# Kernel tuning notes

Hardware: AMD Instinct MI355X
Metric: run time of the kernel (lower is better)

## Reference

```python
import jax, jax.numpy as jnp
import numpy as np

B, L, D = 4, 1024, 512
H, DH = 8, 64
E = 65536  # total subgraph node entries
BN_EPS = 1e-5


def setup_inputs() -> dict:
    key = jax.random.key(0)
    ks = jax.random.split(key, 16)
    x = jax.random.normal(ks[0], (B, L, D), dtype=jnp.float32)
    lattice = jax.random.normal(ks[1], (B, 6), dtype=jnp.float32)  # unused (cond_dim=0)
    B_graph = jax.random.normal(ks[2], (B, L, L), dtype=jnp.float32) * 0.02
    N = B * L
    subgraph_node_index = jax.random.randint(ks[3], (E,), 0, N, dtype=jnp.int32)
    subgraph_indicator = jnp.sort(jax.random.randint(ks[4], (E,), 0, N, dtype=jnp.int32))
    attn_mask = jnp.triu(jnp.ones((L, L), dtype=bool), k=1)  # True = masked (causal)
    s = 0.02
    # Linear weights stored as [in, out]
    Wq = jax.random.normal(ks[5], (D, H * DH), jnp.float32) * s
    Wk = jax.random.normal(ks[6], (D, H * DH), jnp.float32) * s
    Wv = jax.random.normal(ks[7], (D, H * DH), jnp.float32) * s
    Wo = jax.random.normal(ks[8], (H * DH, D), jnp.float32) * s
    bq = jnp.zeros((H * DH,), jnp.float32)
    bk = jnp.zeros((H * DH,), jnp.float32)
    bv = jnp.zeros((H * DH,), jnp.float32)
    bo = jnp.zeros((D,), jnp.float32)
    Wmp = jax.random.normal(ks[9], (D, D), jnp.float32) * s
    bmp = jnp.zeros((D,), jnp.float32)
    bn_gamma = jnp.ones((2 * D,), jnp.float32)
    bn_beta = jnp.zeros((2 * D,), jnp.float32)
    Wex = jax.random.normal(ks[10], (2 * D, D), jnp.float32) * s
    bex = jnp.zeros((D,), jnp.float32)
    struct_scale = jnp.zeros((1,), jnp.float32) + 0.1  # nonzero so bias path is exercised
    return dict(x=x, lattice=lattice, B_graph=B_graph,
                subgraph_node_index=subgraph_node_index,
                subgraph_indicator=subgraph_indicator, attn_mask=attn_mask,
                Wq=Wq, bq=bq, Wk=Wk, bk=bk, Wv=Wv, bv=bv, Wo=Wo, bo=bo,
                Wmp=Wmp, bmp=bmp, bn_gamma=bn_gamma, bn_beta=bn_beta,
                Wex=Wex, bex=bex, struct_scale=struct_scale)


def _extractor(x_flat, sub_idx, sub_ind, Wmp, bmp, bn_gamma, bn_beta, Wex, bex):
    N = x_flat.shape[0]
    x_sub = x_flat[sub_idx]                       # [E, D]
    h = x_sub + (x_sub @ Wmp + bmp)               # 1 message-passing layer (residual)
    # scatter_mean over subgraph_indicator, dim_size=N
    sums = jax.ops.segment_sum(h, sub_ind, num_segments=N)
    cnt = jax.ops.segment_sum(jnp.ones((h.shape[0],), h.dtype), sub_ind, num_segments=N)
    h_pool = sums / jnp.maximum(cnt, 1.0)[:, None]
    out = jnp.concatenate([x_flat, h_pool], axis=-1)  # [N, 2D]
    # BatchNorm1d (training-mode batch stats)
    mu = jnp.mean(out, axis=0)
    var = jnp.var(out, axis=0)
    out = (out - mu) * jax.lax.rsqrt(var + BN_EPS) * bn_gamma + bn_beta
    return out @ Wex + bex                        # [N, D]


def reference(x, lattice, B_graph, subgraph_node_index, subgraph_indicator, attn_mask,
              Wq, bq, Wk, bk, Wv, bv, Wo, bo, Wmp, bmp, bn_gamma, bn_beta,
              Wex, bex, struct_scale):
    Bb, Ll, Dd = x.shape
    scale = 1.0 / np.sqrt(DH).astype(np.float32)
    q = (x @ Wq + bq).reshape(Bb, Ll, H, DH).transpose(0, 2, 1, 3)
    k = (x @ Wk + bk).reshape(Bb, Ll, H, DH).transpose(0, 2, 1, 3)
    v = (x @ Wv + bv).reshape(Bb, Ll, H, DH).transpose(0, 2, 1, 3)
    scores = jnp.einsum('bhqd,bhkd->bhqk', q, k) * scale
    # structural bias from GNN extractor
    x_flat = x.reshape(Bb * Ll, Dd)
    ex = _extractor(x_flat, subgraph_node_index, subgraph_indicator,
                    Wmp, bmp, bn_gamma, bn_beta, Wex, bex)
    x_struct = ex.reshape(Bb, Ll, Dd)
    K = jnp.einsum('bqd,bkd->bqk', x_struct, x_struct) / np.sqrt(Dd).astype(np.float32)
    scores = scores + struct_scale[0] * K[:, None]
    scores = scores + B_graph[:, None]
    mask = attn_mask[None, None]                  # (1,1,L,L), True = masked
    scores = jnp.where(mask, jnp.float32(-10000.0), scores)
    attn = jax.nn.softmax(scores.astype(jnp.float32), axis=-1).astype(scores.dtype)
    # dropout is identity (eval / p effectively 0)
    out = jnp.einsum('bhqk,bhkd->bhqd', attn, v)
    out = out.transpose(0, 2, 1, 3).reshape(Bb, Ll, H * DH)
    out = out @ Wo + bo
    return out, attn
```

## Files before the change

kernel.cpp:

```cpp
#include <hip/hip_runtime.h>
#include <math.h>

#define BB 4
#define LL 1024
#define DD 512
#define HH 8
#define DHH 64
#define EE 65536
#define NNODES 4096
#define HD 512
#define TWO_D 1024

typedef short bf16x8 __attribute__((ext_vector_type(8)));
typedef short short4v __attribute__((ext_vector_type(4)));
typedef float f32x4 __attribute__((ext_vector_type(4)));
typedef unsigned int u32;
#define GL_AS __attribute__((address_space(1)))
#define LDS_AS __attribute__((address_space(3)))

__device__ __forceinline__ short f2bf(float f) {
  u32 u = __builtin_bit_cast(u32, f);
  u = (u + 0x7fffu + ((u >> 16) & 1u)) >> 16;
  return (short)u;
}
__device__ __forceinline__ float b2f(short s) {
  u32 u = ((u32)(unsigned short)s) << 16;
  return __builtin_bit_cast(float, u);
}
__device__ __forceinline__ void gload_lds16(const short* g, short* l) {
  __builtin_amdgcn_global_load_lds((GL_AS const u32*)g, (LDS_AS u32*)l, 16, 0, 0);
}

template <int ROWS>
__device__ __forceinline__ void stage32(const short* g, int lda, short* lds, int tid) {
  const int w = tid >> 6, l = tid & 63;
#pragma unroll
  for (int rep = 0; rep < ROWS / 64; ++rep) {
    const int rbase = rep * 64 + w * 16;
    gload_lds16(g + (size_t)(rbase + (l >> 2)) * lda + (l & 3) * 8, lds + rbase * 32);
  }
}

template <int MREP, int NREP>
__device__ __forceinline__ void mfma_step(const short* As, const short* Bs, int lds_ld, int kofs,
                                          f32x4 (&acc)[MREP][NREP], int wr, int wc, int l) {
  bf16x8 a[MREP], b[NREP];
#pragma unroll
  for (int mi = 0; mi < MREP; ++mi) {
    const int row = wr * (MREP * 16) + mi * 16 + (l & 15);
    a[mi] = *(const bf16x8*)(As + row * lds_ld + kofs + ((l >> 4) << 3));
  }
#pragma unroll
  for (int ni = 0; ni < NREP; ++ni) {
    const int row = wc * (NREP * 16) + ni * 16 + (l & 15);
    b[ni] = *(const bf16x8*)(Bs + row * lds_ld + kofs + ((l >> 4) << 3));
  }
#pragma unroll
  for (int mi = 0; mi < MREP; ++mi)
#pragma unroll
    for (int ni = 0; ni < NREP; ++ni)
      acc[mi][ni] = __builtin_amdgcn_mfma_f32_16x16x32_bf16(a[mi], b[ni], acc[mi][ni], 0, 0, 0);
}

template <int ROWB>
__device__ __forceinline__ bf16x8 ldsw(const short* base, int row, int bir) {
  const int bo = (row * ROWB + bir) ^ ((row & 7) << 4);
  return *(const bf16x8*)((const char*)base + bo);
}

__global__ __launch_bounds__(256) void k_cast_x(const float* __restrict__ x, short* __restrict__ xb) {
  const int i = (blockIdx.x * 256 + threadIdx.x) * 8;
  float4 f0 = *(const float4*)(x + i), f1 = *(const float4*)(x + i + 4);
  bf16x8 s;
  s[0] = f2bf(f0.x); s[1] = f2bf(f0.y); s[2] = f2bf(f0.z); s[3] = f2bf(f0.w);
  s[4] = f2bf(f1.x); s[5] = f2bf(f1.y); s[6] = f2bf(f1.z); s[7] = f2bf(f1.w);
  *(bf16x8*)(xb + i) = s;
}

__global__ __launch_bounds__(256) void k_tcast5(const float* __restrict__ Wq, const float* __restrict__ Wk,
                                                const float* __restrict__ Wv, const float* __restrict__ Wmp,
                                                const float* __restrict__ Wo,
                                                short* __restrict__ WcatT, short* __restrict__ WoT) {
  __shared__ float t[32][33];
  const int zz = blockIdx.z;
  const float* W = (zz == 0) ? Wq : (zz == 1) ? Wk : (zz == 2) ? Wv : (zz == 3) ? Wmp : Wo;
  short* out = (zz < 4) ? (WcatT + zz * 512 * 512) : WoT;
  const int k0 = blockIdx.y * 32, n0 = blockIdx.x * 32;
  const int tx = threadIdx.x, ty = threadIdx.y;
#pragma unroll
  for (int i = 0; i < 4; ++i)
    t[ty + 8 * i][tx] = W[(size_t)(k0 + ty + 8 * i) * 512 + n0 + tx];
  __syncthreads();
#pragma unroll
  for (int i = 0; i < 4; ++i)
    out[(size_t)(n0 + ty + 8 * i) * 512 + k0 + tx] = f2bf(t[tx][ty + 8 * i]);
}

__global__ __launch_bounds__(256) void k_tcast(const float* __restrict__ W, short* __restrict__ out,
                                               int K, int N) {
  __shared__ float t[32][33];
  const int k0 = blockIdx.y * 32, n0 = blockIdx.x * 32;
  const int tx = threadIdx.x, ty = threadIdx.y;
#pragma unroll
  for (int i = 0; i < 4; ++i)
    t[ty + 8 * i][tx] = W[(size_t)(k0 + ty + 8 * i) * N + n0 + tx];
  __syncthreads();
#pragma unroll
  for (int i = 0; i < 4; ++i)
    out[(size_t)(n0 + ty + 8 * i) * K + k0 + tx] = f2bf(t[tx][ty + 8 * i]);
}

__global__ __launch_bounds__(256) void k_pack_bias(const float* bq, const float* bk,
                                                   const float* bv, const float* bmp,
                                                   float* __restrict__ bcat) {
  const int i = blockIdx.x * 256 + threadIdx.x;
  const float* src = (i < 512) ? bq : (i < 1024) ? bk : (i < 1536) ? bv : bmp;
  bcat[i] = src[i & 511];
}

__global__ __launch_bounds__(256) void k_gemm_qkvg(const short* __restrict__ A,
                                                   const short* __restrict__ Bw,
                                                   const float* __restrict__ bcat,
                                                   const float* __restrict__ x,
                                                   short* __restrict__ qT, short* __restrict__ kT,
                                                   short* __restrict__ vT, short* __restrict__ g_bf) {
  __shared__ __align__(16) short As[128 * 32];
  __shared__ __align__(16) short Bs[128 * 32];
  const int tid = threadIdx.x, l = tid & 63, w = tid >> 6, wr = w >> 1, wc = w & 1;
  const int m0 = blockIdx.y * 128, n0 = blockIdx.x * 128;
  f32x4 acc[4][4] = {};
  for (int k0 = 0; k0 < 512; k0 += 32) {
    stage32<128>(A + (size_t)m0 * 512 + k0, 512, As, tid);
    stage32<128>(Bw + (size_t)n0 * 512 + k0, 512, Bs, tid);
    __syncthreads();
    mfma_step<4, 4>(As, Bs, 32, 0, acc, wr, wc, l);
    __syncthreads();
  }
  const int lr = l >> 4, lc = l & 15;
#pragma unroll
  for (int mi = 0; mi < 4; ++mi)
#pragma unroll
    for (int ni = 0; ni < 4; ++ni) {
      const int col = n0 + wc * 64 + ni * 16 + lc;
      const int which = col >> 9;
#pragma unroll
      for (int r = 0; r < 4; ++r) {
        const int row = m0 + wr * 64 + mi * 16 + lr * 4 + r;
        float v = acc[mi][ni][r] + bcat[col];
        if (which < 3) {
          const int hh = (col >> 6) & 7, dh = col & 63;
          const int bb = row >> 10, ll2 = row & 1023;
          short* dst = (which == 0) ? qT : (which == 1) ? kT : vT;
          dst[((size_t)((bb * 8 + hh) * 1024 + ll2)) * 64 + dh] = f2bf(v);
        } else {
          const int c = col & 511;
          g_bf[(size_t)row * 512 + c] = f2bf(v + x[(size_t)row * 512 + c]);
        }
      }
    }
}

__global__ __launch_bounds__(256) void k_gemm_ex(const short* __restrict__ A,
                                                 const short* __restrict__ Bw,
                                                 const float* __restrict__ bias,
                                                 short* __restrict__ C) {
  __shared__ __align__(16) short As[64 * 32];
  __shared__ __align__(16) short Bs[128 * 32];
  const int tid = threadIdx.x, l = tid & 63, w = tid >> 6, wr = w >> 1, wc = w & 1;
  const int m0 = blockIdx.y * 64, n0 = blockIdx.x * 128;
  f32x4 acc[2][4] = {};
  for (int k0 = 0; k0 < 1024; k0 += 32) {
    stage32<64>(A + (size_t)m0 * 1024 + k0, 1024, As, tid);
    stage32<128>(Bw + (size_t)n0 * 1024 + k0, 1024, Bs, tid);
    __syncthreads();
    mfma_step<2, 4>(As, Bs, 32, 0, acc, wr, wc, l);
    __syncthreads();
  }
  const int lr = l >> 4, lc = l & 15;
#pragma unroll
  for (int mi = 0; mi < 2; ++mi)
#pragma unroll
    for (int ni = 0; ni < 4; ++ni) {
      const int col = n0 + wc * 64 + ni * 16 + lc;
      const float bv = bias[col];
#pragma unroll
      for (int r = 0; r < 4; ++r) {
        const int row = m0 + wr * 32 + mi * 16 + lr * 4 + r;
        C[(size_t)row * 512 + col] = f2bf(acc[mi][ni][r] + bv);
      }
    }
}

__global__ __launch_bounds__(256) void k_gemm_oproj(const short* __restrict__ A,
                                                    const short* __restrict__ Bw,
                                                    const float* __restrict__ bias,
                                                    float* __restrict__ C) {
  __shared__ __align__(16) short As[64 * 32];
  __shared__ __align__(16) short Bs[128 * 32];
  const int tid = threadIdx.x, l = tid & 63, w = tid >> 6, wr = w >> 1, wc = w & 1;
  const int m0 = blockIdx.y * 64, n0 = blockIdx.x * 128;
  f32x4 acc[2][4] = {};
  for (int k0 = 0; k0 < 512; k0 += 32) {
    stage32<64>(A + (size_t)m0 * 512 + k0, 512, As, tid);
    stage32<128>(Bw + (size_t)n0 * 512 + k0, 512, Bs, tid);
    __syncthreads();
    mfma_step<2, 4>(As, Bs, 32, 0, acc, wr, wc, l);
    __syncthreads();
  }
  const int lr = l >> 4, lc = l & 15;
#pragma unroll
  for (int mi = 0; mi < 2; ++mi)
#pragma unroll
    for (int ni = 0; ni < 4; ++ni) {
      const int col = n0 + wc * 64 + ni * 16 + lc;
      const float bv = bias[col];
#pragma unroll
      for (int r = 0; r < 4; ++r) {
        const int row = m0 + wr * 32 + mi * 16 + lr * 4 + r;
        C[(size_t)row * 512 + col] = acc[mi][ni][r] + bv;
      }
    }
}

__global__ __launch_bounds__(256) void k_kstruct(const short* __restrict__ ex,
                                                 const float* __restrict__ Bg,
                                                 const float* __restrict__ ssp,
                                                 float* __restrict__ Ksc) {
  const int mt = blockIdx.y, nt = blockIdx.x, b = blockIdx.z;
  if (nt > mt) return;
  __shared__ __align__(16) short As[128 * 32];
  __shared__ __align__(16) short Bs[128 * 32];
  const int tid = threadIdx.x, l = tid & 63, w = tid >> 6, wr = w >> 1, wc = w & 1;
  const int m0 = mt * 128, n0 = nt * 128;
  const short* Az = ex + (size_t)b * 1024 * 512;
  f32x4 acc[4][4] = {};
  for (int k0 = 0; k0 < 512; k0 += 32) {
    stage32<128>(Az + (size_t)m0 * 512 + k0, 512, As, tid);
    stage32<128>(Az + (size_t)n0 * 512 + k0, 512, Bs, tid);
    __syncthreads();
    mfma_step<4, 4>(As, Bs, 32, 0, acc, wr, wc, l);
    __syncthreads();
  }
  const float sc = ssp[0] * 0.04419417382415922f;
  const float* Bgb = Bg + (size_t)b * 1024 * 1024;
  float* Kb = Ksc + (size_t)b * 1024 * 1024;
  const int lr = l >> 4, lc = l & 15;
#pragma unroll
  for (int mi = 0; mi < 4; ++mi)
#pragma unroll
    for (int ni = 0; ni < 4; ++ni) {
      const int col = n0 + wc * 64 + ni * 16 + lc;
#pragma unroll
      for (int r = 0; r < 4; ++r) {
        const int row = m0 + wr * 64 + mi * 16 + lr * 4 + r;
        Kb[(size_t)row * 1024 + col] = fmaf(acc[mi][ni][r], sc, Bgb[(size_t)row * 1024 + col]);
      }
    }
}

__global__ __launch_bounds__(256) void k_attn(const short* __restrict__ qT,
                                              const short* __restrict__ kT,
                                              const short* __restrict__ vT,
                                              const float* __restrict__ Ksc,
                                              float* __restrict__ attn,
                                              short* __restrict__ o_bf) {
  __shared__ __align__(16) short Qs[64 * 64];
  __shared__ __align__(16) short Ks[128 * 64];
  __shared__ __align__(16) short Ps[64 * 128];
  __shared__ __align__(16) short Vls[64 * 128];
  __shared__ float mred[2][64], sred[2][64];

  const int tid = threadIdx.x, l = tid & 63, w = tid >> 6;
  const int wr = w >> 1, wc = w & 1, lr = l >> 4, lc = l & 15;
  const int z = blockIdx.y, b = z >> 3, h = z & 7;
  const int mt = (z & 16) ? (15 - (int)blockIdx.x) : (int)blockIdx.x;
  const int r0 = mt * 64;
  const int NT = (mt + 2) >> 1;

  const short* Qz = qT + (size_t)z * 65536 + (size_t)r0 * 64;
  const short* Kz = kT + (size_t)z * 65536;
  const short* Vz = vT + (size_t)z * 65536;
  const float* Kb = Ksc + (size_t)b * 1048576 + (size_t)r0 * 1024;
  float* Az = attn + (size_t)z * 1048576 + (size_t)r0 * 1024;

#pragma unroll
  for (int rep = 0; rep < 2; ++rep) {
    const int rbase = w * 16 + rep * 8;
    gload_lds16(Qz + (size_t)(rbase + (l >> 3)) * 64 + ((l & 7) ^ (l >> 3)) * 8,
                Qs + rbase * 64);
  }

  const int zc0 = NT * 128;
  if (zc0 < 1024) {
    const int cw = (1024 - zc0) >> 2;
    for (int idx = tid; idx < 64 * cw; idx += 256) {
      const int rowi = idx / cw, c4 = idx - rowi * cw;
      float4 zf = {0.f, 0.f, 0.f, 0.f};
      *(float4*)&Az[(size_t)rowi * 1024 + zc0 + (c4 << 2)] = zf;
    }
  }

  float m8[8], s8[8];
#pragma unroll
  for (int i = 0; i < 8; ++i) { m8[i] = -INFINITY; s8[i] = 0.f; }

  for (int nt = 0; nt < NT; ++nt) {
    const int n0 = nt * 128;
    __syncthreads();
#pragma unroll
    for (int rep = 0; rep < 4; ++rep) {
      const int rbase = rep * 32 + w * 8;
      gload_lds16(Kz + (size_t)(n0 + rbase + (l >> 3)) * 64 + ((l & 7) ^ (l >> 3)) * 8,
                  Ks + rbase * 64);
    }
    __syncthreads();
    f32x4 acc[2][4] = {};
#pragma unroll
    for (int kk = 0; kk < 2; ++kk) {
      const int bir = kk * 64 + lr * 16;
      bf16x8 a[2], bb[4];
#pragma unroll
      for (int mi = 0; mi < 2; ++mi) a[mi] = ldsw<128>(Qs, wr * 32 + mi * 16 + lc, bir);
#pragma unroll
      for (int ni = 0; ni < 4; ++ni) bb[ni] = ldsw<128>(Ks, wc * 64 + ni * 16 + lc, bir);
#pragma unroll
      for (int mi = 0; mi < 2; ++mi)
#pragma unroll
        for (int ni = 0; ni < 4; ++ni)
          acc[mi][ni] = __builtin_amdgcn_mfma_f32_16x16x32_bf16(a[mi], bb[ni], acc[mi][ni], 0, 0, 0);
    }
    const bool lastT = (nt == NT - 1);
#pragma unroll
    for (int mi = 0; mi < 2; ++mi)
#pragma unroll
      for (int rr = 0; rr < 4; ++rr) {
        const int row = wr * 32 + mi * 16 + lr * 4 + rr;
        const int slot = mi * 4 + rr;
        float vals[4], tm = -INFINITY;
#pragma unroll
        for (int ni = 0; ni < 4; ++ni) {
          const int col = wc * 64 + ni * 16 + lc;
          float sc = fmaf(acc[mi][ni][rr], 0.125f, Kb[(size_t)row * 1024 + n0 + col]);
          if (lastT && (n0 + col > r0 + row)) sc = -INFINITY;
          vals[ni] = sc;
          tm = fmaxf(tm, sc);
        }
        if (tm > -INFINITY) {
          const float mn = fmaxf(m8[slot], tm);
          float ts = 0.f;
#pragma unroll
          for (int ni = 0; ni < 4; ++ni) ts += expf(vals[ni] - mn);
          s8[slot] = s8[slot] * expf(m8[slot] - mn) + ts;
          m8[slot] = mn;
        }
      }
  }

#pragma unroll
  for (int off = 1; off < 16; off <<= 1)
#pragma unroll
    for (int i = 0; i < 8; ++i) {
      const float mo = __shfl_xor(m8[i], off, 64);
      const float so = __shfl_xor(s8[i], off, 64);
      const float mn = fmaxf(m8[i], mo);
      if (mn > -INFINITY)
        s8[i] = s8[i] * expf(m8[i] - mn) + so * expf(mo - mn);
      m8[i] = mn;
    }
  if (lc == 0) {
#pragma unroll
    for (int mi = 0; mi < 2; ++mi)
#pragma unroll
      for (int rr = 0; rr < 4; ++rr) {
        const int row = wr * 32 + mi * 16 + lr * 4 + rr;
        mred[wc][row] = m8[mi * 4 + rr];
        sred[wc][row] = s8[mi * 4 + rr];
      }
  }
  __syncthreads();
  float mf[8], inv_s[8];
#pragma unroll
  for (int mi = 0; mi < 2; ++mi)
#pragma unroll
    for (int rr = 0; rr < 4; ++rr) {
      const int row = wr * 32 + mi * 16 + lr * 4 + rr;
      const float ma = mred[0][row], mb = mred[1][row];
      const float mF = fmaxf(ma, mb);
      const float sF = sred[0][row] * expf(ma - mF) + sred[1][row] * expf(mb - mF);
      mf[mi * 4 + rr] = mF;
      inv_s[mi * 4 + rr] = 1.0f / sF;
    }

  f32x4 oacc[4];
#pragma unroll
  for (int i = 0; i < 4; ++i) oacc[i] = f32x4{0.f, 0.f, 0.f, 0.f};

  for (int nt = 0; nt < NT; ++nt) {
    const int n0 = nt * 128;
    __syncthreads();
#pragma unroll
    for (int rep = 0; rep < 4; ++rep) {
      const int rbase = rep * 32 + w * 8;
      gload_lds16(Kz + (size_t)(n0 + rbase + (l >> 3)) * 64 + ((l & 7) ^ (l >> 3)) * 8,
                  Ks + rbase * 64);
    }
    {
      const int j = tid >> 1, d0 = (tid & 1) * 32;
      const short* vsrc = Vz + (size_t)(n0 + j) * 64 + d0;
      bf16x8 v0 = *(const bf16x8*)(vsrc);
      bf16x8 v1 = *(const bf16x8*)(vsrc + 8);
      bf16x8 v2 = *(const bf16x8*)(vsrc + 16);
      bf16x8 v3 = *(const bf16x8*)(vsrc + 24);
#pragma unroll
      for (int i = 0; i < 8; ++i) {
        int dh = d0 + i;
        *(short*)((char*)Vls + ((dh * 256 + j * 2) ^ ((dh & 7) << 4))) = v0[i];
        dh = d0 + 8 + i;
        *(short*)((char*)Vls + ((dh * 256 + j * 2) ^ ((dh & 7) << 4))) = v1[i];
        dh = d0 + 16 + i;
        *(short*)((char*)Vls + ((dh * 256 + j * 2) ^ ((dh & 7) << 4))) = v2[i];
        dh = d0 + 24 + i;
        *(short*)((char*)Vls + ((dh * 256 + j * 2) ^ ((dh & 7) << 4))) = v3[i];
      }
    }
    __syncthreads();
    f32x4 acc[2][4] = {};
#pragma unroll
    for (int kk = 0; kk < 2; ++kk) {
      const int bir = kk * 64 + lr * 16;
      bf16x8 a[2], bb[4];
#pragma unroll
      for (int mi = 0; mi < 2; ++mi) a[mi] = ldsw<128>(Qs, wr * 32 + mi * 16 + lc, bir);
#pragma unroll
      for (int ni = 0; ni < 4; ++ni) bb[ni] = ldsw<128>(Ks, wc * 64 + ni * 16 + lc, bir);
#pragma unroll
      for (int mi = 0; mi < 2; ++mi)
#pragma unroll
        for (int ni = 0; ni < 4; ++ni)
          acc[mi][ni] = __builtin_amdgcn_mfma_f32_16x16x32_bf16(a[mi], bb[ni], acc[mi][ni], 0, 0, 0);
    }
    const bool lastT = (nt == NT - 1);
#pragma unroll
    for (int mi = 0; mi < 2; ++mi)
#pragma unroll
      for (int rr = 0; rr < 4; ++rr) {
        const int row = wr * 32 + mi * 16 + lr * 4 + rr;
        const int slot = mi * 4 + rr;
#pragma unroll
        for (int ni = 0; ni < 4; ++ni) {
          const int col = wc * 64 + ni * 16 + lc;
          const float sc = fmaf(acc[mi][ni][rr], 0.125f, Kb[(size_t)row * 1024 + n0 + col]);
          float p = 0.f;
          if (!(lastT && (n0 + col > r0 + row)))
            p = expf(sc - mf[slot]) * inv_s[slot];
          Az[(size_t)row * 1024 + n0 + col] = p;
          *(short*)((char*)Ps + ((row * 256 + col * 2) ^ ((row & 7) << 4))) = f2bf(p);
        }
      }
    __syncthreads();
#pragma unroll
    for (int ks = 0; ks < 4; ++ks) {
      const int bir = ks * 64 + lr * 16;
      bf16x8 a = ldsw<256>(Ps, w * 16 + lc, bir);
#pragma unroll
      for (int ni = 0; ni < 4; ++ni) {
        bf16x8 bb = ldsw<256>(Vls, ni * 16 + lc, bir);
        oacc[ni] = __builtin_amdgcn_mfma_f32_16x16x32_bf16(a, bb, oacc[ni], 0, 0, 0);
      }
    }
  }

#pragma unroll
  for (int ni = 0; ni < 4; ++ni)
#pragma unroll
    for (int rr = 0; rr < 4; ++rr) {
      const int row = r0 + w * 16 + lr * 4 + rr;
      const int dh = ni * 16 + lc;
      o_bf[((size_t)(b * 1024 + row)) * 512 + h * 64 + dh] = f2bf(oacc[ni][rr]);
    }
}

__global__ __launch_bounds__(128) void k_segmean(const short* __restrict__ g,
                                                 const int* __restrict__ idx,
                                                 const int* __restrict__ ind,
                                                 float* __restrict__ hp) {
  __shared__ int sh[2];
  const int s = blockIdx.x;
  if (threadIdx.x == 0) {
    int lo = 0, hi = EE;
    while (lo < hi) { int mid = (lo + hi) >> 1; if (ind[mid] < s) lo = mid + 1; else hi = mid; }
    sh[0] = lo;
    int lo2 = lo, hi2 = EE;
    while (lo2 < hi2) { int mid = (lo2 + hi2) >> 1; if (ind[mid] <= s) lo2 = mid + 1; else hi2 = mid; }
    sh[1] = lo2;
  }
  __syncthreads();
  const int lo = sh[0], hi = sh[1];
  const int d0 = threadIdx.x << 2;
  float a0 = 0.f, a1 = 0.f, a2 = 0.f, a3 = 0.f;
  for (int e = lo; e < hi; ++e) {
    const short4v v = *(const short4v*)(g + (size_t)idx[e] * 512 + d0);
    a0 += b2f(v[0]); a1 += b2f(v[1]); a2 += b2f(v[2]); a3 += b2f(v[3]);
  }
  const float ic = (hi > lo) ? 1.0f / (float)(hi - lo) : 0.0f;
  float4 o = {a0 * ic, a1 * ic, a2 * ic, a3 * ic};
  *(float4*)(hp + (size_t)s * 512 + d0) = o;
}

__global__ __launch_bounds__(256) void k_stats1(const float* __restrict__ x,
                                                const float* __restrict__ hp,
                                                float* __restrict__ scr) {
  const int blk = blockIdx.x, tid = threadIdx.x;
  const int c = tid * 2, r0 = blk * 128;
  float sx0 = 0, sx1 = 0, qx0 = 0, qx1 = 0, sh0 = 0, sh1 = 0, qh0 = 0, qh1 = 0;
  for (int r = 0; r < 128; ++r) {
    const size_t off = (size_t)(r0 + r) * 512 + c;
    float2 vx = *(const float2*)(x + off);
    float2 vh = *(const float2*)(hp + off);
    sx0 += vx.x; sx1 += vx.y; qx0 = fmaf(vx.x, vx.x, qx0); qx1 = fmaf(vx.y, vx.y, qx1);
    sh0 += vh.x; sh1 += vh.y; qh0 = fmaf(vh.x, vh.x, qh0); qh1 = fmaf(vh.y, vh.y, qh1);
  }
  float* p = scr + (size_t)blk * 4096;
  p[c] = sx0; p[c + 1] = sx1;
  p[512 + c] = sh0; p[512 + c + 1] = sh1;
  p[2048 + c] = qx0; p[2048 + c + 1] = qx1;
  p[2048 + 512 + c] = qh0; p[2048 + 512 + c + 1] = qh1;
}
__global__ __launch_bounds__(128) void k_stats2(const float* __restrict__ scr,
                                                float* __restrict__ mu, float* __restrict__ inv) {
  const int f = blockIdx.x * 128 + threadIdx.x;
  float s = 0.f, q = 0.f;
  for (int i = 0; i < 32; ++i) {
    s += scr[(size_t)i * 4096 + f];
    q += scr[(size_t)i * 4096 + 2048 + f];
  }
  const float m = s * (1.0f / NNODES);
  mu[f] = m;
  inv[f] = rsqrtf(q * (1.0f / NNODES) - m * m + 1e-5f);
}

__global__ __launch_bounds__(256) void k_norm(const float* __restrict__ x,
                                              const float* __restrict__ hp,
                                              const float* __restrict__ mu,
                                              const float* __restrict__ inv,
                                              const float* __restrict__ gamma,
                                              const float* __restrict__ beta,
                                              short* __restrict__ nrm) {
  const int gid = blockIdx.x * 256 + threadIdx.x;
  const int n = gid >> 8, f = (gid & 255) << 2;
  float4 v = (f < 512) ? *(const float4*)(x + (size_t)n * 512 + f)
                       : *(const float4*)(hp + (size_t)n * 512 + (f - 512));
  short4v o;
  o[0] = f2bf((v.x - mu[f + 0]) * inv[f + 0] * gamma[f + 0] + beta[f + 0]);
  o[1] = f2bf((v.y - mu[f + 1]) * inv[f + 1] * gamma[f + 1] + beta[f + 1]);
  o[2] = f2bf((v.z - mu[f + 2]) * inv[f + 2] * gamma[f + 2] + beta[f + 2]);
  o[3] = f2bf((v.w - mu[f + 3]) * inv[f + 3] * gamma[f + 3] + beta[f + 3]);
  *(short4v*)(nrm + (size_t)n * 1024 + f) = o;
}

extern "C" void kernel_launch(void* const* d_in, const int* in_sizes, int n_in,
                              void* d_out, int out_size, void* d_ws, size_t ws_size,
                              hipStream_t stream) {
  const float* x     = (const float*)d_in[0];
  const float* Bg    = (const float*)d_in[2];
  const int*   sidx  = (const int*)d_in[3];
  const int*   sind  = (const int*)d_in[4];
  const float* Wq    = (const float*)d_in[6];
  const float* bq    = (const float*)d_in[7];
  const float* Wk    = (const float*)d_in[8];
  const float* bk    = (const float*)d_in[9];
  const float* Wv    = (const float*)d_in[10];
  const float* bv    = (const float*)d_in[11];
  const float* Wo    = (const float*)d_in[12];
  const float* bo    = (const float*)d_in[13];
  const float* Wmp   = (const float*)d_in[14];
  const float* bmp   = (const float*)d_in[15];
  const float* gamma = (const float*)d_in[16];
  const float* beta  = (const float*)d_in[17];
  const float* Wex   = (const float*)d_in[18];
  const float* bex   = (const float*)d_in[19];
  const float* ssp   = (const float*)d_in[20];

  char* W = (char*)d_ws;
  short* x_bf  = (short*)(W + 0);
  short* WcatT = (short*)(W + 4194304);
  short* WexT  = (short*)(W + 6291456);
  short* WoT   = (short*)(W + 7340032);
  float* bcat  = (float*)(W + 7864320);
  short* qT    = (short*)(W + 7872512);
  short* kT    = (short*)(W + 12066816);
  short* vT    = (short*)(W + 16261120);
  short* g_bf  = (short*)(W + 20455424);
  float* hp    = (float*)(W + 24649728);
  short* nrm   = (short*)(W + 33038336);
  short* ex_bf = (short*)(W + 41426944);
  float* Ksc   = (float*)(W + 45621248);
  short* o_bf  = (short*)(W + 62398464);
  float* scr   = (float*)(W + 66592768);
  float* muv   = (float*)(W + 67117056);
  float* invv  = (float*)(W + 67121152);

  float* outp = (float*)d_out;
  float* attn = outp + (size_t)BB * LL * HD;

  dim3 t256(256), t32x8(32, 8);

  k_cast_x<<<dim3(1024), t256, 0, stream>>>(x, x_bf);
  k_tcast5<<<dim3(16, 16, 5), t32x8, 0, stream>>>(Wq, Wk, Wv, Wmp, Wo, WcatT, WoT);
  k_tcast<<<dim3(16, 32), t32x8, 0, stream>>>(Wex, WexT, 1024, 512);
  k_pack_bias<<<dim3(8), t256, 0, stream>>>(bq, bk, bv, bmp, bcat);

  k_gemm_qkvg<<<dim3(16, 32), t256, 0, stream>>>(x_bf, WcatT, bcat, x, qT, kT, vT, g_bf);

  k_segmean<<<dim3(NNODES), dim3(128), 0, stream>>>(g_bf, sidx, sind, hp);
  k_stats1<<<dim3(32), t256, 0, stream>>>(x, hp, scr);
  k_stats2<<<dim3(8), dim3(128), 0, stream>>>(scr, muv, invv);
  k_norm<<<dim3(4096), t256, 0, stream>>>(x, hp, muv, invv, gamma, beta, nrm);
  k_gemm_ex<<<dim3(4, 64), t256, 0, stream>>>(nrm, WexT, bex, ex_bf);

  k_kstruct<<<dim3(8, 8, 4), t256, 0, stream>>>(ex_bf, Bg, ssp, Ksc);

  k_attn<<<dim3(16, 32), t256, 0, stream>>>(qT, kT, vT, Ksc, attn, o_bf);

  k_gemm_oproj<<<dim3(4, 64), t256, 0, stream>>>(o_bf, WoT, bo, outp);
}
```

Measured before the change: 421.8 us.

## Shrink attention tiles, pre-transpose V, and fold log2e into scores for exp2

Result: faster. 395.7 us (-6.2%).

```diff
diff --git a/kernel.cpp b/kernel.cpp
--- a/kernel.cpp
+++ b/kernel.cpp
@@ -116,6 +116,30 @@
   const int i = blockIdx.x * 256 + threadIdx.x;
   const float* src = (i < 512) ? bq : (i < 1024) ? bk : (i < 1536) ? bv : bmp;
   bcat[i] = src[i & 511];
+}
+
+__global__ __launch_bounds__(256) void k_vtt(const short* __restrict__ vT, short* __restrict__ vTT) {
+  __shared__ short t[64][65];
+  const int z = blockIdx.y, j0 = blockIdx.x * 64;
+  const short* src = vT + (size_t)z * 65536;
+  short* dst = vTT + (size_t)z * 65536;
+  const int tid = threadIdx.x;
+  const int jr = tid >> 3, c0 = (tid & 7) * 8;
+#pragma unroll
+  for (int rep = 0; rep < 2; ++rep) {
+    bf16x8 v = *(const bf16x8*)(src + (size_t)(j0 + jr + rep * 32) * 64 + c0);
+#pragma unroll
+    for (int i = 0; i < 8; ++i) t[jr + rep * 32][c0 + i] = v[i];
+  }
+  __syncthreads();
+#pragma unroll
+  for (int rep = 0; rep < 2; ++rep) {
+    const int d = (tid >> 3) + rep * 32;
+    bf16x8 o;
+#pragma unroll
+    for (int i = 0; i < 8; ++i) o[i] = t[c0 + i][d];
+    *(bf16x8*)(dst + (size_t)d * 1024 + j0 + c0) = o;
+  }
 }
 
 __global__ __launch_bounds__(256) void k_gemm_qkvg(const short* __restrict__ A,
@@ -241,7 +265,8 @@
     mfma_step<4, 4>(As, Bs, 32, 0, acc, wr, wc, l);
     __syncthreads();
   }
-  const float sc = ssp[0] * 0.04419417382415922f;
+  const float l2e = 1.4426950408889634f;
+  const float sc = ssp[0] * 0.04419417382415922f * l2e;
   const float* Bgb = Bg + (size_t)b * 1024 * 1024;
   float* Kb = Ksc + (size_t)b * 1024 * 1024;
   const int lr = l >> 4, lc = l & 15;
@@ -253,229 +278,187 @@
 #pragma unroll
       for (int r = 0; r < 4; ++r) {
         const int row = m0 + wr * 64 + mi * 16 + lr * 4 + r;
-        Kb[(size_t)row * 1024 + col] = fmaf(acc[mi][ni][r], sc, Bgb[(size_t)row * 1024 + col]);
-      }
-    }
-}
+        Kb[(size_t)row * 1024 + col] =
+            fmaf(acc[mi][ni][r], sc, Bgb[(size_t)row * 1024 + col] * l2e);
+      }
+    }
+}
+
+#define QSC 0.18033688011112042f
 
 __global__ __launch_bounds__(256) void k_attn(const short* __restrict__ qT,
                                               const short* __restrict__ kT,
-                                              const short* __restrict__ vT,
+                                              const short* __restrict__ vTT,
                                               const float* __restrict__ Ksc,
                                               float* __restrict__ attn,
                                               short* __restrict__ o_bf) {
-  __shared__ __align__(16) short Qs[64 * 64];
-  __shared__ __align__(16) short Ks[128 * 64];
-  __shared__ __align__(16) short Ps[64 * 128];
-  __shared__ __align__(16) short Vls[64 * 128];
-  __shared__ float mred[2][64], sred[2][64];
+  __shared__ __align__(16) short Qs[32 * 64];
+  __shared__ __align__(16) short Ks[64 * 64];
+  __shared__ __align__(16) short Ps[32 * 64];
+  __shared__ __align__(16) short Vls[64 * 64];
+  __shared__ float mred[2][32], sred[2][32];
 
   const int tid = threadIdx.x, l = tid & 63, w = tid >> 6;
   const int wr = w >> 1, wc = w & 1, lr = l >> 4, lc = l & 15;
   const int z = blockIdx.y, b = z >> 3, h = z & 7;
-  const int mt = (z & 16) ? (15 - (int)blockIdx.x) : (int)blockIdx.x;
-  const int r0 = mt * 64;
-  const int NT = (mt + 2) >> 1;
+  const int mt = (z & 16) ? (31 - (int)blockIdx.x) : (int)blockIdx.x;
+  const int r0 = mt * 32;
+  const int NT = (mt >> 1) + 1;
 
   const short* Qz = qT + (size_t)z * 65536 + (size_t)r0 * 64;
   const short* Kz = kT + (size_t)z * 65536;
-  const short* Vz = vT + (size_t)z * 65536;
+  const short* Vz = vTT + (size_t)z * 65536;
   const float* Kb = Ksc + (size_t)b * 1048576 + (size_t)r0 * 1024;
   float* Az = attn + (size_t)z * 1048576 + (size_t)r0 * 1024;
 
-#pragma unroll
-  for (int rep = 0; rep < 2; ++rep) {
-    const int rbase = w * 16 + rep * 8;
+  {
+    const int rbase = w * 8;
     gload_lds16(Qz + (size_t)(rbase + (l >> 3)) * 64 + ((l & 7) ^ (l >> 3)) * 8,
                 Qs + rbase * 64);
   }
 
-  const int zc0 = NT * 128;
+  const int zc0 = NT * 64;
   if (zc0 < 1024) {
     const int cw = (1024 - zc0) >> 2;
-    for (int idx = tid; idx < 64 * cw; idx += 256) {
+    for (int idx = tid; idx < 32 * cw; idx += 256) {
       const int rowi = idx / cw, c4 = idx - rowi * cw;
       float4 zf = {0.f, 0.f, 0.f, 0.f};
       *(float4*)&Az[(size_t)rowi * 1024 + zc0 + (c4 << 2)] = zf;
     }
   }
 
-  float m8[8], s8[8];
-#pragma unroll
-  for (int i = 0; i < 8; ++i) { m8[i] = -INFINITY; s8[i] = 0.f; }
+  float m2[4], s2[4];
+#pragma unroll
+  for (int i = 0; i < 4; ++i) { m2[i] = -INFINITY; s2[i] = 0.f; }
 
   for (int nt = 0; nt < NT; ++nt) {
-    const int n0 = nt * 128;
-    __syncthreads();
-#pragma unroll
-    for (int rep = 0; rep < 4; ++rep) {
+    const int n0 = nt * 64;
+    __syncthreads();
+#pragma unroll
+    for (int rep = 0; rep < 2; ++rep) {
       const int rbase = rep * 32 + w * 8;
       gload_lds16(Kz + (size_t)(n0 + rbase + (l >> 3)) * 64 + ((l & 7) ^ (l >> 3)) * 8,
                   Ks + rbase * 64);
     }
     __syncthreads();
-    f32x4 acc[2][4] = {};
+    f32x4 acc[2] = {};
 #pragma unroll
     for (int kk = 0; kk < 2; ++kk) {
       const int bir = kk * 64 + lr * 16;
-      bf16x8 a[2], bb[4];
-#pragma unroll
-      for (int mi = 0; mi < 2; ++mi) a[mi] = ldsw<128>(Qs, wr * 32 + mi * 16 + lc, bir);
-#pragma unroll
-      for (int ni = 0; ni < 4; ++ni) bb[ni] = ldsw<128>(Ks, wc * 64 + ni * 16 + lc, bir);
-#pragma unroll
-      for (int mi = 0; mi < 2; ++mi)
-#pragma unroll
-        for (int ni = 0; ni < 4; ++ni)
-          acc[mi][ni] = __builtin_amdgcn_mfma_f32_16x16x32_bf16(a[mi], bb[ni], acc[mi][ni], 0, 0, 0);
-    }
-    const bool lastT = (nt == NT - 1);
-#pragma unroll
-    for (int mi = 0; mi < 2; ++mi)
-#pragma unroll
-      for (int rr = 0; rr < 4; ++rr) {
-        const int row = wr * 32 + mi * 16 + lr * 4 + rr;
-        const int slot = mi * 4 + rr;
-        float vals[4], tm = -INFINITY;
-#pragma unroll
-        for (int ni = 0; ni < 4; ++ni) {
-          const int col = wc * 64 + ni * 16 + lc;
-          float sc = fmaf(acc[mi][ni][rr], 0.125f, Kb[(size_t)row * 1024 + n0 + col]);
-          if (lastT && (n0 + col > r0 + row)) sc = -INFINITY;
-          vals[ni] = sc;
-          tm = fmaxf(tm, sc);
-        }
-        if (tm > -INFINITY) {
-          const float mn = fmaxf(m8[slot], tm);
-          float ts = 0.f;
-#pragma unroll
-          for (int ni = 0; ni < 4; ++ni) ts += expf(vals[ni] - mn);
-          s8[slot] = s8[slot] * expf(m8[slot] - mn) + ts;
-          m8[slot] = mn;
-        }
-      }
+      bf16x8 a = ldsw<128>(Qs, wr * 16 + lc, bir);
+#pragma unroll
+      for (int ni = 0; ni < 2; ++ni) {
+        bf16x8 bb = ldsw<128>(Ks, wc * 32 + ni * 16 + lc, bir);
+        acc[ni] = __builtin_amdgcn_mfma_f32_16x16x32_bf16(a, bb, acc[ni], 0, 0, 0);
+      }
+    }
+#pragma unroll
+    for (int rr = 0; rr < 4; ++rr) {
+      const int rowl = wr * 16 + lr * 4 + rr;
+      float vals[2], tm = -INFINITY;
+#pragma unroll
+      for (int ni = 0; ni < 2; ++ni) {
+        const int coll = wc * 32 + ni * 16 + lc;
+        float sc = fmaf(acc[ni][rr], QSC, Kb[(size_t)rowl * 1024 + n0 + coll]);
+        if (n0 + coll > r0 + rowl) sc = -INFINITY;
+        vals[ni] = sc;
+        tm = fmaxf(tm, sc);
+      }
+      if (tm > -INFINITY) {
+        const float mn = fmaxf(m2[rr], tm);
+        s2[rr] = s2[rr] * exp2f(m2[rr] - mn) + exp2f(vals[0] - mn) + exp2f(vals[1] - mn);
+        m2[rr] = mn;
+      }
+    }
   }
 
 #pragma unroll
   for (int off = 1; off < 16; off <<= 1)
 #pragma unroll
-    for (int i = 0; i < 8; ++i) {
-      const float mo = __shfl_xor(m8[i], off, 64);
-      const float so = __shfl_xor(s8[i], off, 64);
-      const float mn = fmaxf(m8[i], mo);
+    for (int i = 0; i < 4; ++i) {
+      const float mo = __shfl_xor(m2[i], off, 64);
+      const float so = __shfl_xor(s2[i], off, 64);
+      const float mn = fmaxf(m2[i], mo);
       if (mn > -INFINITY)
-        s8[i] = s8[i] * expf(m8[i] - mn) + so * expf(mo - mn);
-      m8[i] = mn;
+        s2[i] = s2[i] * exp2f(m2[i] - mn) + so * exp2f(mo - mn);
+      m2[i] = mn;
     }
   if (lc == 0) {
 #pragma unroll
-    for (int mi = 0; mi < 2; ++mi)
-#pragma unroll
-      for (int rr = 0; rr < 4; ++rr) {
-        const int row = wr * 32 + mi * 16 + lr * 4 + rr;
-        mred[wc][row] = m8[mi * 4 + rr];
-        sred[wc][row] = s8[mi * 4 + rr];
-      }
+    for (int rr = 0; rr < 4; ++rr) {
+      const int rowl = wr * 16 + lr * 4 + rr;
+      mred[wc][rowl] = m2[rr];
+      sred[wc][rowl] = s2[rr];
+    }
   }
   __syncthreads();
-  float mf[8], inv_s[8];
-#pragma unroll
-  for (int mi = 0; mi < 2; ++mi)
-#pragma unroll
-    for (int rr = 0; rr < 4; ++rr) {
-      const int row = wr * 32 + mi * 16 + lr * 4 + rr;
-      const float ma = mred[0][row], mb = mred[1][row];
-      const float mF = fmaxf(ma, mb);
-      const float sF = sred[0][row] * expf(ma - mF) + sred[1][row] * expf(mb - mF);
-      mf[mi * 4 + rr] = mF;
-      inv_s[mi * 4 + rr] = 1.0f / sF;
-    }
-
-  f32x4 oacc[4];
-#pragma unroll
-  for (int i = 0; i < 4; ++i) oacc[i] = f32x4{0.f, 0.f, 0.f, 0.f};
-
+  float mfv[4], invs[4];
+#pragma unroll
+  for (int rr = 0; rr < 4; ++rr) {
+    const int rowl = wr * 16 + lr * 4 + rr;
+    const float ma = mred[0][rowl], mb = mred[1][rowl];
+    const float mF = fmaxf(ma, mb);
+    const float sF = sred[0][rowl] * exp2f(ma - mF) + sred[1][rowl] * exp2f(mb - mF);
+    mfv[rr] = mF;
+    invs[rr] = 1.0f / sF;
+  }
+
+  f32x4 oacc[2] = {};
   for (int nt = 0; nt < NT; ++nt) {
-    const int n0 = nt * 128;
-    __syncthreads();
-#pragma unroll
-    for (int rep = 0; rep < 4; ++rep) {
+    const int n0 = nt * 64;
+    __syncthreads();
+#pragma unroll
+    for (int rep = 0; rep < 2; ++rep) {
       const int rbase = rep * 32 + w * 8;
       gload_lds16(Kz + (size_t)(n0 + rbase + (l >> 3)) * 64 + ((l & 7) ^ (l >> 3)) * 8,
                   Ks + rbase * 64);
-    }
-    {
-      const int j = tid >> 1, d0 = (tid & 1) * 32;
-      const short* vsrc = Vz + (size_t)(n0 + j) * 64 + d0;
-      bf16x8 v0 = *(const bf16x8*)(vsrc);
-      bf16x8 v1 = *(const bf16x8*)(vsrc + 8);
-      bf16x8 v2 = *(const bf16x8*)(vsrc + 16);
-      bf16x8 v3 = *(const bf16x8*)(vsrc + 24);
-#pragma unroll
-      for (int i = 0; i < 8; ++i) {
-        int dh = d0 + i;
-        *(short*)((char*)Vls + ((dh * 256 + j * 2) ^ ((dh & 7) << 4))) = v0[i];
-        dh = d0 + 8 + i;
-        *(short*)((char*)Vls + ((dh * 256 + j * 2) ^ ((dh & 7) << 4))) = v1[i];
-        dh = d0 + 16 + i;
-        *(short*)((char*)Vls + ((dh * 256 + j * 2) ^ ((dh & 7) << 4))) = v2[i];
-        dh = d0 + 24 + i;
-        *(short*)((char*)Vls + ((dh * 256 + j * 2) ^ ((dh & 7) << 4))) = v3[i];
-      }
-    }
-    __syncthreads();
-    f32x4 acc[2][4] = {};
+      gload_lds16(Vz + (size_t)(rbase + (l >> 3)) * 1024 + n0 + ((l & 7) ^ (l >> 3)) * 8,
+                  Vls + rbase * 64);
+    }
+    __syncthreads();
+    f32x4 acc[2] = {};
 #pragma unroll
     for (int kk = 0; kk < 2; ++kk) {
       const int bir = kk * 64 + lr * 16;
-      bf16x8 a[2], bb[4];
-#pragma unroll
-      for (int mi = 0; mi < 2; ++mi) a[mi] = ldsw<128>(Qs, wr * 32 + mi * 16 + lc, bir);
-#pragma unroll
-      for (int ni = 0; ni < 4; ++ni) bb[ni] = ldsw<128>(Ks, wc * 64 + ni * 16 + lc, bir);
-#pragma unroll
-      for (int mi = 0; mi < 2; ++mi)
-#pragma unroll
-        for (int ni = 0; ni < 4; ++ni)
-          acc[mi][ni] = __builtin_amdgcn_mfma_f32_16x16x32_bf16(a[mi], bb[ni], acc[mi][ni], 0, 0, 0);
-    }
-    const bool lastT = (nt == NT - 1);
-#pragma unroll
-    for (int mi = 0; mi < 2; ++mi)
-#pragma unroll
-      for (int rr = 0; rr < 4; ++rr) {
-        const int row = wr * 32 + mi * 16 + lr * 4 + rr;
-        const int slot = mi * 4 + rr;
-#pragma unroll
-        for (int ni = 0; ni < 4; ++ni) {
-          const int col = wc * 64 + ni * 16 + lc;
-          const float sc = fmaf(acc[mi][ni][rr], 0.125f, Kb[(size_t)row * 1024 + n0 + col]);
-          float p = 0.f;
-          if (!(lastT && (n0 + col > r0 + row)))
-            p = expf(sc - mf[slot]) * inv_s[slot];
-          Az[(size_t)row * 1024 + n0 + col] = p;
-          *(short*)((char*)Ps + ((row * 256 + col * 2) ^ ((row & 7) << 4))) = f2bf(p);
-        }
-      }
-    __syncthreads();
-#pragma unroll
-    for (int ks = 0; ks < 4; ++ks) {
-      const int bir = ks * 64 + lr * 16;
-      bf16x8 a = ldsw<256>(Ps, w * 16 + lc, bir);
-#pragma unroll
-      for (int ni = 0; ni < 4; ++ni) {
-        bf16x8 bb = ldsw<256>(Vls, ni * 16 + lc, bir);
+      bf16x8 a = ldsw<128>(Qs, wr * 16 + lc, bir);
+#pragma unroll
+      for (int ni = 0; ni < 2; ++ni) {
+        bf16x8 bb = ldsw<128>(Ks, wc * 32 + ni * 16 + lc, bir);
+        acc[ni] = __builtin_amdgcn_mfma_f32_16x16x32_bf16(a, bb, acc[ni], 0, 0, 0);
+      }
+    }
+#pragma unroll
+    for (int rr = 0; rr < 4; ++rr) {
+      const int rowl = wr * 16 + lr * 4 + rr;
+#pragma unroll
+      for (int ni = 0; ni < 2; ++ni) {
+        const int coll = wc * 32 + ni * 16 + lc;
+        const float sc = fmaf(acc[ni][rr], QSC, Kb[(size_t)rowl * 1024 + n0 + coll]);
+        float p = 0.f;
+        if (n0 + coll <= r0 + rowl) p = exp2f(sc - mfv[rr]) * invs[rr];
+        Az[(size_t)rowl * 1024 + n0 + coll] = p;
+        *(short*)((char*)Ps + ((rowl * 128 + coll * 2) ^ ((rowl & 7) << 4))) = f2bf(p);
+      }
+    }
+    __syncthreads();
+#pragma unroll
+    for (int kk = 0; kk < 2; ++kk) {
+      const int bir = kk * 64 + lr * 16;
+      bf16x8 a = ldsw<128>(Ps, wr * 16 + lc, bir);
+#pragma unroll
+      for (int ni = 0; ni < 2; ++ni) {
+        bf16x8 bb = ldsw<128>(Vls, wc * 32 + ni * 16 + lc, bir);
         oacc[ni] = __builtin_amdgcn_mfma_f32_16x16x32_bf16(a, bb, oacc[ni], 0, 0, 0);
       }
     }
   }
 
 #pragma unroll
-  for (int ni = 0; ni < 4; ++ni)
+  for (int ni = 0; ni < 2; ++ni)
 #pragma unroll
     for (int rr = 0; rr < 4; ++rr) {
-      const int row = r0 + w * 16 + lr * 4 + rr;
-      const int dh = ni * 16 + lc;
+      const int row = r0 + wr * 16 + lr * 4 + rr;
+      const int dh = wc * 32 + ni * 16 + lc;
       o_bf[((size_t)(b * 1024 + row)) * 512 + h * 64 + dh] = f2bf(oacc[ni][rr]);
     }
 }
@@ -599,6 +582,7 @@
   float* scr   = (float*)(W + 66592768);
   float* muv   = (float*)(W + 67117056);
   float* invv  = (float*)(W + 67121152);
+  short* vTT   = (short*)(W + 67125248);
 
   float* outp = (float*)d_out;
   float* attn = outp + (size_t)BB * LL * HD;
@@ -611,6 +595,7 @@
   k_pack_bias<<<dim3(8), t256, 0, stream>>>(bq, bk, bv, bmp, bcat);
 
   k_gemm_qkvg<<<dim3(16, 32), t256, 0, stream>>>(x_bf, WcatT, bcat, x, qT, kT, vT, g_bf);
+  k_vtt<<<dim3(16, 32), t256, 0, stream>>>(vT, vTT);
 
   k_segmean<<<dim3(NNODES), dim3(128), 0, stream>>>(g_bf, sidx, sind, hp);
   k_stats1<<<dim3(32), t256, 0, stream>>>(x, hp, scr);
@@ -620,7 +605,7 @@
 
   k_kstruct<<<dim3(8, 8, 4), t256, 0, stream>>>(ex_bf, Bg, ssp, Ksc);
 
-  k_attn<<<dim3(16, 32), t256, 0, stream>>>(qT, kT, vT, Ksc, attn, o_bf);
+  k_attn<<<dim3(32, 32), t256, 0, stream>>>(qT, kT, vTT, Ksc, attn, o_bf);
 
   k_gemm_oproj<<<dim3(4, 64), t256, 0, stream>>>(o_bf, WoT, bo, outp);
 }
```
